# Optimization experiments

Hardware: AMD Instinct MI355X
Metric: run time of the kernel (lower is better)

Reference implementation:

```python
import jax, jax.numpy as jnp
import numpy as np

B, L, D, N_HEADS = 4, 8192, 1024, 16
HD = D // N_HEADS
MASK_NEG = -1e10


def setup_inputs() -> dict:
    key = jax.random.key(0)
    ks = jax.random.split(key, 5)
    # xavier_normal std for square Dense: sqrt(2/(fan_in+fan_out))
    std = (2.0 / (D + D)) ** 0.5
    return {
        "query": jax.random.normal(ks[0], (B, L, D), dtype=jnp.float32),
        "mask": jax.random.bernoulli(ks[1], 0.1, (B, L)),  # True = masked out
        "Wq": std * jax.random.normal(ks[2], (D, D), dtype=jnp.float32),
        "bq": jnp.zeros((D,), dtype=jnp.float32),
        "Wk": std * jax.random.normal(ks[3], (D, D), dtype=jnp.float32),
        "bk": jnp.zeros((D,), dtype=jnp.float32),
        "Wv": std * jax.random.normal(ks[4], (D, D), dtype=jnp.float32),
        "bv": jnp.zeros((D,), dtype=jnp.float32),
    }


def reference(query, mask, Wq, bq, Wk, bk, Wv, bv):
    # Self-attention: key = value = query (original falls back when key/value are None)
    q = query @ Wq + bq  # [B, L, D]
    k = query @ Wk + bk
    v = query @ Wv + bv
    # split heads: b l (n h) -> b l n h
    qs = q.reshape(B, L, N_HEADS, HD)
    ks_ = k.reshape(B, L, N_HEADS, HD)
    vs = v.reshape(B, L, N_HEADS, HD)
    m = mask[:, :, None, None]  # [B, L, 1, 1], broadcast over heads & dims
    K = jnp.where(m, MASK_NEG, ks_)
    V = jnp.where(m, 0.0, vs)
    # elu kernel feature map: phi(x) = elu(x) + 1 (elu(-1e10)+1 -> 0 for masked keys)
    phiK = jax.nn.elu(K) + 1.0
    phiQ = jax.nn.elu(qs) + 1.0
    # per-head kv summary: [B, N, HD_k, HD_v]
    kv = jnp.einsum('blnk,blnv->bnkv', phiK, V)
    # FAITHFUL to original einsum 'blk,bkv->blk': sums kv over v, elementwise with phiQ
    kv_sum = kv.sum(-1)  # [B, N, HD]
    out = phiQ * kv_sum[:, None, :, :]  # [B, L, N, HD]
    # combine heads: b l n h -> b l (n h)
    return out.reshape(B, L, D)
```

## Files before the change

kernel.cpp:

```cpp
#include <hip/hip_runtime.h>

typedef unsigned short u16;
typedef unsigned int u32;
typedef __attribute__((ext_vector_type(8))) short s16x8;
typedef __attribute__((ext_vector_type(4))) float f32x4;

#define GAS __attribute__((address_space(1)))
#define LAS __attribute__((address_space(3)))

#define BB 4
#define LL 8192
#define DD 1024
#define NH 16
#define HD 64
#define MROWS (BB * LL)
#define NWBT 2064

__device__ __forceinline__ u16 f2bf(float f) {
  u32 u = __builtin_bit_cast(u32, f);
  u32 r = (u + 0x7FFFu + ((u >> 16) & 1u)) >> 16;
  return (u16)r;
}
__device__ __forceinline__ float bf2f(u32 lo) {
  return __builtin_bit_cast(float, lo << 16);
}

__device__ __forceinline__ void async16(const void* g, void* l) {
  __builtin_amdgcn_global_load_lds((const GAS u32*)g, (LAS u32*)l, 16, 0, 0);
}

__device__ __forceinline__ bool get_mask(const void* mp, int row, int mode) {
  if (mode == 2) return ((const unsigned char*)mp)[row] != 0;
  if (mode == 1) return ((const float*)mp)[row] != 0.f;
  return ((const int*)mp)[row] != 0;
}

__global__ void build_wbt(const float* __restrict__ Wq, const float* __restrict__ Wk,
                          u16* __restrict__ WbT) {
  __shared__ float t[32][33];
  const int n0 = blockIdx.x * 32;
  const int k0 = blockIdx.y * 32;
  const float* W = (n0 >> 10) == 0 ? Wq : Wk;
  const int nloc = n0 & 1023;
  const int tx = threadIdx.x, ty = threadIdx.y;
#pragma unroll
  for (int j = 0; j < 32; j += 8)
    t[ty + j][tx] = W[(size_t)(k0 + ty + j) * DD + nloc + tx];
  __syncthreads();
#pragma unroll
  for (int j = 0; j < 32; j += 8)
    WbT[(size_t)(n0 + ty + j) * DD + k0 + tx] = f2bf(t[tx][ty + j]);
}

__global__ void build_aux(const float* __restrict__ Wv, const float* __restrict__ bq,
                          const float* __restrict__ bk, const float* __restrict__ bv,
                          const u32* __restrict__ m,
                          u16* __restrict__ WbT, float* __restrict__ bcat,
                          int* __restrict__ flag) {
  const int blk = blockIdx.x;
  const int tid = threadIdx.x;
  if (blk < 64) {
    int i = blk * 256 + tid;
    int k = i >> 4, h = i & 15;
    float s = 0.f;
    const float* p = Wv + (size_t)k * DD + h * HD;
#pragma unroll 8
    for (int j = 0; j < 64; ++j) s += p[j];
    WbT[(size_t)(2048 + h) * DD + k] = f2bf(s);
  } else if (blk < 73) {
    int i = (blk - 64) * 256 + tid;
    if (i < 1024) bcat[i] = bq[i];
    else if (i < 2048) bcat[i] = bk[i - 1024];
    else if (i < 2064) {
      float s = 0.f;
      const float* p = bv + (i - 2048) * HD;
#pragma unroll 8
      for (int j = 0; j < 64; ++j) s += p[j];
      bcat[i] = s;
    }
  } else {
    int i = (blk - 73) * 256 + tid;
    u32 v = m[i];
    int f = 0;
    if (v == 0x3F800000u) f = 1;
    else if (v > 1u) f = 2;
    if (f) atomicMax(flag, f);
  }
}

__global__ __launch_bounds__(256) void prep_q(
    const float* __restrict__ query, const u16* __restrict__ WbT,
    const float* __restrict__ bcat, const void* __restrict__ maskp,
    const int* __restrict__ mmode,
    u16* __restrict__ qb, float* __restrict__ sV) {
  __shared__ float sVp[2][16][16];
  const int tid = threadIdx.x;
  const int lane = tid & 63;
  const int w = tid >> 6;
  const int wl = w >> 1;
  const int ks = w & 1;
  const int l15 = lane & 15, l16 = lane >> 4;
  const int row0 = blockIdx.x * 32 + wl * 16;
  const int arow = row0 + l15;

  const float* qrow = query + (size_t)arow * DD + ks * 512 + l16 * 8;
  u16* qbrow = qb + (size_t)arow * DD + ks * 512 + l16 * 8;
  const u16* wrow = WbT + (size_t)(2048 + l15) * DD + ks * 512 + l16 * 8;

  f32x4 acc = {};
#pragma unroll
  for (int mac = 0; mac < 2; ++mac) {
    float4 qv[16];
    s16x8 wv[8];
#pragma unroll
    for (int s = 0; s < 8; ++s) {
      const int off = mac * 256 + s * 32;
      qv[s * 2] = *(const float4*)(qrow + off);
      qv[s * 2 + 1] = *(const float4*)(qrow + off + 4);
      wv[s] = *(const s16x8*)(wrow + off);
    }
#pragma unroll
    for (int s = 0; s < 8; ++s) {
      s16x8 o;
      o[0] = (short)f2bf(qv[s * 2].x);     o[1] = (short)f2bf(qv[s * 2].y);
      o[2] = (short)f2bf(qv[s * 2].z);     o[3] = (short)f2bf(qv[s * 2].w);
      o[4] = (short)f2bf(qv[s * 2 + 1].x); o[5] = (short)f2bf(qv[s * 2 + 1].y);
      o[6] = (short)f2bf(qv[s * 2 + 1].z); o[7] = (short)f2bf(qv[s * 2 + 1].w);
      *(s16x8*)(qbrow + mac * 256 + s * 32) = o;
      acc = __builtin_amdgcn_mfma_f32_16x16x32_bf16(o, wv[s], acc, 0, 0, 0);
    }
  }

  if (ks == 1) {
#pragma unroll
    for (int r = 0; r < 4; ++r) sVp[wl][l16 * 4 + r][l15] = acc[r];
  }
  __syncthreads();
  if (ks == 0) {
    const int mode = *mmode;
#pragma unroll
    for (int r = 0; r < 4; ++r) {
      const int row = row0 + l16 * 4 + r;
      const bool msk = get_mask(maskp, row, mode);
      float v = acc[r] + sVp[wl][l16 * 4 + r][l15] + bcat[2048 + l15];
      sV[(size_t)row * NH + l15] = msk ? 0.f : v;
    }
  }
}

#define BUFSZ 8192
#define UOFF(buf, mat, ks) (((((buf)*2 + (mat))*2 + (ks))) * BUFSZ)

__global__ __launch_bounds__(512, 2) void gemm_qkv(
    const u16* __restrict__ qb, const u16* __restrict__ WbT,
    const float* __restrict__ bcat, const void* __restrict__ maskp,
    const int* __restrict__ mmode,
    const float* __restrict__ sV, float* __restrict__ kv,
    float* __restrict__ out, int phase) {
  __shared__ __align__(16) u16 lds[65536];
  const int tid = threadIdx.x;
  const int lane = tid & 63;
  const int w = tid >> 6;
  const int wm = w & 1, wn = w >> 1;
  const int l15 = lane & 15, l16 = lane >> 4;

  const int bid = blockIdx.x;
  const int swz = (bid & 7) * 64 + (bid >> 3);
  const int mt = swz >> 2;
  const int nt = swz & 3;
  const int row0 = mt * 256;
  const int col0 = (phase ? 1024 : 0) + nt * 256;

  f32x4 acc[8][4] = {};

#define STAGE(buf, mat, ks, kt) do {                                        \
    const u16* gb_ = (mat) ? (WbT + (size_t)col0 * DD)                      \
                           : (qb + (size_t)row0 * DD);                      \
    const int kt_ = (kt) & 15;                                              \
    _Pragma("unroll")                                                       \
    for (int j_ = 0; j_ < 2; ++j_) {                                        \
      int li_ = tid + j_ * 512;                                             \
      int row_ = li_ >> 2, slot_ = li_ & 3;                                 \
      int c_ = slot_ ^ ((row_ >> 1) & 3);                                   \
      async16(gb_ + (size_t)row_ * DD + kt_ * 64 + (ks) * 32 + c_ * 8,      \
              lds + UOFF(buf, mat, ks) + li_ * 8);                          \
    }                                                                       \
  } while (0)

#define LDA(buf, ks, a) do {                                                \
    _Pragma("unroll")                                                       \
    for (int mi_ = 0; mi_ < 8; ++mi_) {                                     \
      int r_ = wm * 128 + mi_ * 16 + l15;                                   \
      a[mi_] = *(const s16x8*)(lds + UOFF(buf, 0, ks) + r_ * 32 +           \
                               ((l16 ^ ((r_ >> 1) & 3)) * 8));              \
    }                                                                       \
  } while (0)

#define LDB2(buf, ks, nb, b) do {                                           \
    _Pragma("unroll")                                                       \
    for (int q_ = 0; q_ < 2; ++q_) {                                        \
      int r_ = wn * 64 + ((nb)*2 + q_) * 16 + l15;                          \
      b[q_] = *(const s16x8*)(lds + UOFF(buf, 1, ks) + r_ * 32 +            \
                              ((l16 ^ ((r_ >> 1) & 3)) * 8));               \
    }                                                                       \
  } while (0)

#define MM(a, b, nb) do {                                                   \
    __builtin_amdgcn_s_setprio(1);                                          \
    _Pragma("unroll")                                                       \
    for (int mi_ = 0; mi_ < 8; ++mi_) {                                     \
      acc[mi_][(nb)*2] = __builtin_amdgcn_mfma_f32_16x16x32_bf16(           \
          a[mi_], b[0], acc[mi_][(nb)*2], 0, 0, 0);                         \
      acc[mi_][(nb)*2 + 1] = __builtin_amdgcn_mfma_f32_16x16x32_bf16(       \
          a[mi_], b[1], acc[mi_][(nb)*2 + 1], 0, 0, 0);                     \
    }                                                                       \
    __builtin_amdgcn_s_setprio(0);                                          \
  } while (0)

#define BAR() __builtin_amdgcn_s_barrier()
#define VMW6() asm volatile("s_waitcnt vmcnt(6)" ::: "memory")

  STAGE(0, 0, 0, 0); STAGE(0, 1, 0, 0); STAGE(0, 0, 1, 0); STAGE(0, 1, 1, 0);
  STAGE(1, 0, 0, 1); STAGE(1, 1, 0, 1); STAGE(1, 0, 1, 1);
  VMW6();
  BAR();

  for (int t = 0; t < 16; t += 2) {
    s16x8 a[8], b[2];
    LDA(0, 0, a); LDB2(0, 0, 0, b);
    STAGE(1, 1, 1, t + 1);
    BAR(); MM(a, b, 0); BAR();
    LDB2(0, 0, 1, b);
    STAGE(0, 0, 0, t + 2);
    BAR(); MM(a, b, 1); BAR();
    LDA(0, 1, a); LDB2(0, 1, 0, b);
    STAGE(0, 1, 0, t + 2);
    BAR(); MM(a, b, 0); BAR();
    LDB2(0, 1, 1, b);
    STAGE(0, 0, 1, t + 2);
    BAR(); MM(a, b, 1); VMW6(); BAR();
    LDA(1, 0, a); LDB2(1, 0, 0, b);
    STAGE(0, 1, 1, t + 2);
    BAR(); MM(a, b, 0); BAR();
    LDB2(1, 0, 1, b);
    STAGE(1, 0, 0, t + 3);
    BAR(); MM(a, b, 1); BAR();
    LDA(1, 1, a); LDB2(1, 1, 0, b);
    STAGE(1, 1, 0, t + 3);
    BAR(); MM(a, b, 0); BAR();
    LDB2(1, 1, 1, b);
    STAGE(1, 0, 1, t + 3);
    BAR(); MM(a, b, 1); VMW6(); BAR();
  }

  const int mode = *mmode;
  const int lanec = lane & 15, laneq = lane >> 4;
  const int wcol0 = col0 + wn * 64;
  const int b_ = row0 >> 13;

  if (phase == 1) {
    const int n = (wcol0 - 1024) >> 6;
    float pc[4] = {0.f, 0.f, 0.f, 0.f};
#pragma unroll
    for (int mi = 0; mi < 8; ++mi) {
#pragma unroll
      for (int r = 0; r < 4; ++r) {
        const int row = row0 + wm * 128 + mi * 16 + laneq * 4 + r;
        const bool msk = get_mask(maskp, row, mode);
        if (!msk) {
          const float sv = sV[(size_t)row * NH + n];
#pragma unroll
          for (int ni = 0; ni < 4; ++ni) {
            const int col = wcol0 + ni * 16 + lanec;
            float v = acc[mi][ni][r] + bcat[col];
            float phi = v > 0.f ? v + 1.f : __expf(v);
            pc[ni] += phi * sv;
          }
        }
      }
    }
#pragma unroll
    for (int ni = 0; ni < 4; ++ni) {
      pc[ni] += __shfl_xor(pc[ni], 16);
      pc[ni] += __shfl_xor(pc[ni], 32);
    }
    if (laneq == 0) {
#pragma unroll
      for (int ni = 0; ni < 4; ++ni) {
        const int colk = wcol0 - 1024 + ni * 16 + lanec;
        atomicAdd(&kv[b_ * DD + colk], pc[ni]);
      }
    }
  } else {
    float kvv[4];
#pragma unroll
    for (int ni = 0; ni < 4; ++ni)
      kvv[ni] = kv[b_ * DD + wcol0 + ni * 16 + lanec];
#pragma unroll
    for (int mi = 0; mi < 8; ++mi) {
#pragma unroll
      for (int r = 0; r < 4; ++r) {
        const int row = row0 + wm * 128 + mi * 16 + laneq * 4 + r;
#pragma unroll
        for (int ni = 0; ni < 4; ++ni) {
          const int col = wcol0 + ni * 16 + lanec;
          float v = acc[mi][ni][r] + bcat[col];
          float phi = v > 0.f ? v + 1.f : __expf(v);
          out[(size_t)row * DD + col] = phi * kvv[ni];
        }
      }
    }
  }
}

extern "C" void kernel_launch(void* const* d_in, const int* in_sizes, int n_in,
                              void* d_out, int out_size, void* d_ws, size_t ws_size,
                              hipStream_t stream) {
  const float* query = (const float*)d_in[0];
  const void* maskp = d_in[1];
  const float* Wq = (const float*)d_in[2];
  const float* bq = (const float*)d_in[3];
  const float* Wk = (const float*)d_in[4];
  const float* bk = (const float*)d_in[5];
  const float* Wv = (const float*)d_in[6];
  const float* bv = (const float*)d_in[7];
  float* out = (float*)d_out;

  char* ws = (char*)d_ws;
  u16* qb = (u16*)ws;            ws += (size_t)MROWS * DD * 2;
  u16* WbT = (u16*)ws;           ws += (size_t)NWBT * DD * 2;
  float* sV = (float*)ws;        ws += (size_t)MROWS * NH * 4;
  float* bcat = (float*)ws;      ws += (size_t)NWBT * 4;
  float* kv = (float*)ws;        ws += (size_t)BB * DD * 4;
  int* mflag = (int*)ws;         ws += 256;

  hipMemsetAsync(kv, 0, (size_t)BB * DD * 4 + 256, stream);

  build_wbt<<<dim3(2048 / 32, DD / 32), dim3(32, 8), 0, stream>>>(Wq, Wk, WbT);
  build_aux<<<105, 256, 0, stream>>>(Wv, bq, bk, bv, (const u32*)maskp, WbT, bcat, mflag);
  prep_q<<<MROWS / 32, 256, 0, stream>>>(query, WbT, bcat, maskp, mflag, qb, sV);
  gemm_qkv<<<512, 512, 0, stream>>>(qb, WbT, bcat, maskp, mflag, sV, kv, out, 1);
  gemm_qkv<<<512, 512, 0, stream>>>(qb, WbT, bcat, maskp, mflag, sV, kv, out, 0);
}
```

Measured before the change: 412.1 us.

## Halve GEMM M-tile to 128 rows and shrink LDS for higher occupancy

Reduces the QKV GEMM block tile from 256x256 to 128x256 rows and switches from 64-wide K stages split into two halves to single 32-wide K stages double-buffered in about 48KB of LDS. The grid doubles to 1024 blocks and launch bounds ask for 4 blocks per CU, so more waves can hide latency and the work spreads over more CUs. In exchange, arithmetic intensity per block drops, B tiles are loaded twice as often, and barriers per K-step increase. The pipeline is rewritten with a peeled final iteration and new vmcnt waits.

Result: no change. 410.5 us (-0.4%).

```diff
diff --git a/kernel.cpp b/kernel.cpp
--- a/kernel.cpp
+++ b/kernel.cpp
@@ -148,16 +148,16 @@
   }
 }
 
-#define BUFSZ 8192
-#define UOFF(buf, mat, ks) (((((buf)*2 + (mat))*2 + (ks))) * BUFSZ)
-
-__global__ __launch_bounds__(512, 2) void gemm_qkv(
+#define AOFF(buf) ((buf) * 12288)
+#define BOFF(buf) ((buf) * 12288 + 4096)
+
+__global__ __launch_bounds__(512, 4) void gemm_qkv(
     const u16* __restrict__ qb, const u16* __restrict__ WbT,
     const float* __restrict__ bcat, const void* __restrict__ maskp,
     const int* __restrict__ mmode,
     const float* __restrict__ sV, float* __restrict__ kv,
     float* __restrict__ out, int phase) {
-  __shared__ __align__(16) u16 lds[65536];
+  __shared__ __align__(16) u16 lds[24576];
   const int tid = threadIdx.x;
   const int lane = tid & 63;
   const int w = tid >> 6;
@@ -165,42 +165,46 @@
   const int l15 = lane & 15, l16 = lane >> 4;
 
   const int bid = blockIdx.x;
-  const int swz = (bid & 7) * 64 + (bid >> 3);
+  const int swz = (bid & 7) * 128 + (bid >> 3);
   const int mt = swz >> 2;
   const int nt = swz & 3;
-  const int row0 = mt * 256;
+  const int row0 = mt * 128;
   const int col0 = (phase ? 1024 : 0) + nt * 256;
 
-  f32x4 acc[8][4] = {};
-
-#define STAGE(buf, mat, ks, kt) do {                                        \
-    const u16* gb_ = (mat) ? (WbT + (size_t)col0 * DD)                      \
-                           : (qb + (size_t)row0 * DD);                      \
-    const int kt_ = (kt) & 15;                                              \
+  f32x4 acc[4][4] = {};
+
+#define STAGE_A(buf, kt) do {                                               \
+    int row_ = tid >> 2, slot_ = tid & 3;                                   \
+    int c_ = slot_ ^ ((row_ >> 1) & 3);                                     \
+    async16(qb + (size_t)(row0 + row_) * DD + (kt) * 32 + c_ * 8,           \
+            lds + AOFF(buf) + tid * 8);                                     \
+  } while (0)
+
+#define STAGE_B(buf, kt) do {                                               \
     _Pragma("unroll")                                                       \
     for (int j_ = 0; j_ < 2; ++j_) {                                        \
       int li_ = tid + j_ * 512;                                             \
       int row_ = li_ >> 2, slot_ = li_ & 3;                                 \
       int c_ = slot_ ^ ((row_ >> 1) & 3);                                   \
-      async16(gb_ + (size_t)row_ * DD + kt_ * 64 + (ks) * 32 + c_ * 8,      \
-              lds + UOFF(buf, mat, ks) + li_ * 8);                          \
+      async16(WbT + (size_t)(col0 + row_) * DD + (kt) * 32 + c_ * 8,        \
+              lds + BOFF(buf) + li_ * 8);                                   \
     }                                                                       \
   } while (0)
 
-#define LDA(buf, ks, a) do {                                                \
+#define LDA(buf, a) do {                                                    \
     _Pragma("unroll")                                                       \
-    for (int mi_ = 0; mi_ < 8; ++mi_) {                                     \
-      int r_ = wm * 128 + mi_ * 16 + l15;                                   \
-      a[mi_] = *(const s16x8*)(lds + UOFF(buf, 0, ks) + r_ * 32 +           \
+    for (int mi_ = 0; mi_ < 4; ++mi_) {                                     \
+      int r_ = wm * 64 + mi_ * 16 + l15;                                    \
+      a[mi_] = *(const s16x8*)(lds + AOFF(buf) + r_ * 32 +                  \
                                ((l16 ^ ((r_ >> 1) & 3)) * 8));              \
     }                                                                       \
   } while (0)
 
-#define LDB2(buf, ks, nb, b) do {                                           \
+#define LDB2(buf, nb, b) do {                                               \
     _Pragma("unroll")                                                       \
     for (int q_ = 0; q_ < 2; ++q_) {                                        \
       int r_ = wn * 64 + ((nb)*2 + q_) * 16 + l15;                          \
-      b[q_] = *(const s16x8*)(lds + UOFF(buf, 1, ks) + r_ * 32 +            \
+      b[q_] = *(const s16x8*)(lds + BOFF(buf) + r_ * 32 +                   \
                               ((l16 ^ ((r_ >> 1) & 3)) * 8));               \
     }                                                                       \
   } while (0)
@@ -208,7 +212,7 @@
 #define MM(a, b, nb) do {                                                   \
     __builtin_amdgcn_s_setprio(1);                                          \
     _Pragma("unroll")                                                       \
-    for (int mi_ = 0; mi_ < 8; ++mi_) {                                     \
+    for (int mi_ = 0; mi_ < 4; ++mi_) {                                     \
       acc[mi_][(nb)*2] = __builtin_amdgcn_mfma_f32_16x16x32_bf16(           \
           a[mi_], b[0], acc[mi_][(nb)*2], 0, 0, 0);                         \
       acc[mi_][(nb)*2 + 1] = __builtin_amdgcn_mfma_f32_16x16x32_bf16(       \
@@ -218,39 +222,41 @@
   } while (0)
 
 #define BAR() __builtin_amdgcn_s_barrier()
-#define VMW6() asm volatile("s_waitcnt vmcnt(6)" ::: "memory")
-
-  STAGE(0, 0, 0, 0); STAGE(0, 1, 0, 0); STAGE(0, 0, 1, 0); STAGE(0, 1, 1, 0);
-  STAGE(1, 0, 0, 1); STAGE(1, 1, 0, 1); STAGE(1, 0, 1, 1);
-  VMW6();
+#define VMW1() asm volatile("s_waitcnt vmcnt(1)" ::: "memory")
+#define VMW3() asm volatile("s_waitcnt vmcnt(3)" ::: "memory")
+#define VMW0() asm volatile("s_waitcnt vmcnt(0)" ::: "memory")
+
+  STAGE_A(0, 0); STAGE_B(0, 0); STAGE_A(1, 1); STAGE_B(1, 1);
+  VMW3();
   BAR();
 
-  for (int t = 0; t < 16; t += 2) {
-    s16x8 a[8], b[2];
-    LDA(0, 0, a); LDB2(0, 0, 0, b);
-    STAGE(1, 1, 1, t + 1);
+  for (int t = 0; t < 30; t += 2) {
+    s16x8 a[4], b[2];
+    LDA(0, a); LDB2(0, 0, b);
+    if (t > 0) STAGE_B(1, t + 1);
     BAR(); MM(a, b, 0); BAR();
-    LDB2(0, 0, 1, b);
-    STAGE(0, 0, 0, t + 2);
-    BAR(); MM(a, b, 1); BAR();
-    LDA(0, 1, a); LDB2(0, 1, 0, b);
-    STAGE(0, 1, 0, t + 2);
+    LDB2(0, 1, b);
+    STAGE_A(0, t + 2);
+    BAR(); MM(a, b, 1); VMW1(); BAR();
+    LDA(1, a); LDB2(1, 0, b);
+    STAGE_B(0, t + 2);
     BAR(); MM(a, b, 0); BAR();
-    LDB2(0, 1, 1, b);
-    STAGE(0, 0, 1, t + 2);
-    BAR(); MM(a, b, 1); VMW6(); BAR();
-    LDA(1, 0, a); LDB2(1, 0, 0, b);
-    STAGE(0, 1, 1, t + 2);
+    LDB2(1, 1, b);
+    STAGE_A(1, t + 3);
+    BAR(); MM(a, b, 1); VMW1(); BAR();
+  }
+
+  {
+    s16x8 a[4], b[2];
+    LDA(0, a); LDB2(0, 0, b);
+    STAGE_B(1, 31);
     BAR(); MM(a, b, 0); BAR();
-    LDB2(1, 0, 1, b);
-    STAGE(1, 0, 0, t + 3);
-    BAR(); MM(a, b, 1); BAR();
-    LDA(1, 1, a); LDB2(1, 1, 0, b);
-    STAGE(1, 1, 0, t + 3);
+    LDB2(0, 1, b);
+    BAR(); MM(a, b, 1); VMW0(); BAR();
+    LDA(1, a); LDB2(1, 0, b);
     BAR(); MM(a, b, 0); BAR();
-    LDB2(1, 1, 1, b);
-    STAGE(1, 0, 1, t + 3);
-    BAR(); MM(a, b, 1); VMW6(); BAR();
+    LDB2(1, 1, b);
+    BAR(); MM(a, b, 1);
   }
 
   const int mode = *mmode;
@@ -262,10 +268,10 @@
     const int n = (wcol0 - 1024) >> 6;
     float pc[4] = {0.f, 0.f, 0.f, 0.f};
 #pragma unroll
-    for (int mi = 0; mi < 8; ++mi) {
+    for (int mi = 0; mi < 4; ++mi) {
 #pragma unroll
       for (int r = 0; r < 4; ++r) {
-        const int row = row0 + wm * 128 + mi * 16 + laneq * 4 + r;
+        const int row = row0 + wm * 64 + mi * 16 + laneq * 4 + r;
         const bool msk = get_mask(maskp, row, mode);
         if (!msk) {
           const float sv = sV[(size_t)row * NH + n];
@@ -297,10 +303,10 @@
     for (int ni = 0; ni < 4; ++ni)
       kvv[ni] = kv[b_ * DD + wcol0 + ni * 16 + lanec];
 #pragma unroll
-    for (int mi = 0; mi < 8; ++mi) {
+    for (int mi = 0; mi < 4; ++mi) {
 #pragma unroll
       for (int r = 0; r < 4; ++r) {
-        const int row = row0 + wm * 128 + mi * 16 + laneq * 4 + r;
+        const int row = row0 + wm * 64 + mi * 16 + laneq * 4 + r;
 #pragma unroll
         for (int ni = 0; ni < 4; ++ni) {
           const int col = wcol0 + ni * 16 + lanec;
@@ -339,6 +345,6 @@
   build_wbt<<<dim3(2048 / 32, DD / 32), dim3(32, 8), 0, stream>>>(Wq, Wk, WbT);
   build_aux<<<105, 256, 0, stream>>>(Wv, bq, bk, bv, (const u32*)maskp, WbT, bcat, mflag);
   prep_q<<<MROWS / 32, 256, 0, stream>>>(query, WbT, bcat, maskp, mflag, qb, sV);
-  gemm_qkv<<<512, 512, 0, stream>>>(qb, WbT, bcat, maskp, mflag, sV, kv, out, 1);
-  gemm_qkv<<<512, 512, 0, stream>>>(qb, WbT, bcat, maskp, mflag, sV, kv, out, 0);
-}
+  gemm_qkv<<<1024, 512, 0, stream>>>(qb, WbT, bcat, maskp, mflag, sV, kv, out, 1);
+  gemm_qkv<<<1024, 512, 0, stream>>>(qb, WbT, bcat, maskp, mflag, sV, kv, out, 0);
+}
```
